# Kernel optimization log

Measured on AMD Instinct MI355X. Metric: run time of the kernel, lower is better.

Reference implementation:

```python
import jax, jax.numpy as jnp
import numpy as np

B, C, H, W = 2, 256, 64, 64
D = 4  # max dilation ring


def _offsets():
    offs = [(0, 0)]
    for s in range(1, D + 1):
        for a in (-s, 0, s):
            for b in (-s, 0, s):
                if a != 0 or b != 0:
                    offs.append((a, b))
    return np.array(offs, dtype=np.int32)  # (33, 2)


def setup_inputs() -> dict:
    key = jax.random.key(0)
    k1, k2, k3, k4 = jax.random.split(key, 4)
    scale = 1.0 / np.sqrt(C)
    return {
        "Ft": jax.random.normal(k1, (B, C, H, W), dtype=jnp.float32),
        "Ft_epsilon": jax.random.normal(k2, (B, C, H, W), dtype=jnp.float32),
        "Wf": jax.random.normal(k3, (256, C), dtype=jnp.float32) * scale,
        "bf": jnp.zeros((256,), dtype=jnp.float32),
        "Wg": jax.random.normal(k4, (256, C), dtype=jnp.float32) * scale,
        "bg": jnp.zeros((256,), dtype=jnp.float32),
    }


def reference(Ft, Ft_epsilon, Wf, bf, Wg, bg):
    # 1x1 conv embeddings
    Ef = jnp.einsum("bchw,oc->bohw", Ft, Wf) + bf[None, :, None, None]          # f(Ft)
    Eg = jnp.einsum("bchw,oc->bohw", Ft_epsilon, Wg) + bg[None, :, None, None]  # g(Ft_eps)

    offs = _offsets()                                  # (K,2), K=33
    dx = jnp.asarray(offs[:, 0])[:, None, None]        # (K,1,1)
    dy = jnp.asarray(offs[:, 1])[:, None, None]
    xs = jnp.arange(H)[None, :, None] + dx             # (K,H,1)
    ys = jnp.arange(W)[None, None, :] + dy             # (K,1,W)
    valid = ((xs >= 0) & (xs < H)) & ((ys >= 0) & (ys < W))  # (K,H,W)
    xc = jnp.clip(xs, 0, H - 1)
    yc = jnp.clip(ys, 0, W - 1)

    # gather neighbor embeddings and features: (B,C,K,H,W)
    Ef_n = Ef[:, :, xc, yc]
    Ft_n = Ft[:, :, xc, yc]

    # affinity of center embedding with each neighbor embedding
    aff = jnp.einsum("bchw,bckhw->bkhw", Eg, Ef_n)     # (B,K,H,W)
    aff = jnp.where(valid[None], aff, -jnp.inf)        # clip out-of-bounds neighbors
    w = jax.nn.softmax(aff, axis=1)                    # (B,K,H,W); center always valid

    out = jnp.einsum("bkhw,bckhw->bchw", w, Ft_n)      # (B,C,H,W)
    return out
```

## Files before the change

### kernel.cpp

```cpp
#include <hip/hip_runtime.h>
#include <math.h>

typedef __attribute__((ext_vector_type(4))) float f4;

__device__ __forceinline__ int iclamp(int x, int lo, int hi) { return min(max(x, lo), hi); }

__device__ constexpr int DXC[33] = {0, -1,-1,-1,0,0,1,1,1, -2,-2,-2,0,0,2,2,2, -3,-3,-3,0,0,3,3,3, -4,-4,-4,0,0,4,4,4};
__device__ constexpr int DYC[33] = {0, -1,0,1,-1,1,-1,0,1, -2,0,2,-2,2,-2,0,2, -3,0,3,-3,3,-3,0,3, -4,0,4,-4,4,-4,0,4};

__global__ __launch_bounds__(256) void mat_M(
    const float* __restrict__ Wf, const float* __restrict__ Wg,
    const float* __restrict__ bg, float* __restrict__ M, float* __restrict__ r)
{
    __shared__ float Sf[32][33], Sg[32][33];
    __shared__ float Rs[32][9];
    const int c1b = blockIdx.x * 32, c2b = blockIdx.y * 32;
    const int tid = threadIdx.x;
    const int tx = tid & 15, ty = tid >> 4;
    float acc[2][2] = {};
    for (int ko = 0; ko < 256; ko += 32) {
        #pragma unroll
        for (int i = 0; i < 4; ++i) {
            int f = i * 256 + tid;
            int o = f >> 5, c = f & 31;
            Sf[o][c] = Wf[(ko + o) * 256 + c1b + c];
            Sg[o][c] = Wg[(ko + o) * 256 + c2b + c];
        }
        __syncthreads();
        #pragma unroll
        for (int o = 0; o < 32; ++o) {
            float f0 = Sf[o][ty * 2], f1 = Sf[o][ty * 2 + 1];
            float g0 = Sg[o][tx * 2], g1 = Sg[o][tx * 2 + 1];
            acc[0][0] += f0 * g0; acc[0][1] += f0 * g1;
            acc[1][0] += f1 * g0; acc[1][1] += f1 * g1;
        }
        __syncthreads();
    }
    #pragma unroll
    for (int i = 0; i < 2; ++i)
        #pragma unroll
        for (int j = 0; j < 2; ++j)
            M[(size_t)(c1b + ty * 2 + i) * 256 + c2b + tx * 2 + j] = acc[i][j];

    if (blockIdx.y == 0) {
        const int c1l = tid & 31, og = tid >> 5;
        float s = 0.f;
        #pragma unroll 8
        for (int o = og * 32; o < og * 32 + 32; ++o)
            s += Wf[o * 256 + c1b + c1l] * bg[o];
        Rs[c1l][og] = s;
        __syncthreads();
        if (tid < 32) {
            float t = 0.f;
            #pragma unroll
            for (int j = 0; j < 8; ++j) t += Rs[tid][j];
            r[c1b + tid] = t;
        }
    }
}

__global__ __launch_bounds__(256, 2) void gemm_G(
    const float* __restrict__ M, const float* __restrict__ r,
    const float* __restrict__ X0, float* __restrict__ G)
{
    __shared__ float As[2][32][132];
    __shared__ float Bs[2][32][64];

    const int bn = blockIdx.x, bm = blockIdx.y, b = blockIdx.z;
    const float* X = X0 + (size_t)b * 256 * 4096;
    float* E = G + (size_t)b * 256 * 4096;

    const int tid = threadIdx.x;
    const int tn = tid & 15, tm = tid >> 4;
    const int m0 = bm * 128, n0 = bn * 64;

    float acc[8][4] = {};
    f4 areg[4], breg[2];

    auto loadA = [&](int kk) {
        #pragma unroll
        for (int i = 0; i < 4; ++i) {
            int f = i * 256 + tid, m = f >> 3, cq = f & 7;
            areg[i] = *(const f4*)&M[(m0 + m) * 256 + kk + cq * 4];
        }
    };
    auto loadB = [&](int kk) {
        #pragma unroll
        for (int i = 0; i < 2; ++i) {
            int f = i * 256 + tid, c = f >> 4, n4 = f & 15;
            breg[i] = *(const f4*)&X[(size_t)(kk + c) * 4096 + n0 + n4 * 4];
        }
    };
    auto storeLDS = [&](int buf) {
        #pragma unroll
        for (int i = 0; i < 4; ++i) {
            int f = i * 256 + tid, m = f >> 3, cq = f & 7;
            As[buf][cq * 4 + 0][m] = areg[i].x;
            As[buf][cq * 4 + 1][m] = areg[i].y;
            As[buf][cq * 4 + 2][m] = areg[i].z;
            As[buf][cq * 4 + 3][m] = areg[i].w;
        }
        #pragma unroll
        for (int i = 0; i < 2; ++i) {
            int f = i * 256 + tid, c = f >> 4, n4 = f & 15;
            *(f4*)&Bs[buf][c][n4 * 4] = breg[i];
        }
    };

    loadA(0); loadB(0); storeLDS(0);
    __syncthreads();

    for (int ch = 0; ch < 8; ++ch) {
        const int buf = ch & 1;
        if (ch < 7) { loadA((ch + 1) * 32); loadB((ch + 1) * 32); }
        #pragma unroll 4
        for (int k = 0; k < 32; ++k) {
            f4 a0 = *(const f4*)&As[buf][k][tm * 8];
            f4 a1 = *(const f4*)&As[buf][k][tm * 8 + 4];
            f4 bb = *(const f4*)&Bs[buf][k][tn * 4];
            #pragma unroll
            for (int ii = 0; ii < 4; ++ii)
                #pragma unroll
                for (int jj = 0; jj < 4; ++jj) {
                    acc[ii][jj]     += a0[ii] * bb[jj];
                    acc[4 + ii][jj] += a1[ii] * bb[jj];
                }
        }
        if (ch < 7) storeLDS(buf ^ 1);
        __syncthreads();
    }

    #pragma unroll
    for (int rr = 0; rr < 8; ++rr) {
        int o = m0 + tm * 8 + rr;
        float bvs = r[o];
        f4 v = { acc[rr][0] + bvs, acc[rr][1] + bvs, acc[rr][2] + bvs, acc[rr][3] + bvs };
        *(f4*)&E[(size_t)o * 4096 + n0 + tn * 4] = v;
    }
}

template<int K0, int NK>
__device__ __forceinline__ void aff_accum(const float* __restrict__ base, float* __restrict__ aff)
{
    #pragma unroll
    for (int ch = 0; ch < 8; ++ch) {
        float eg = base[(72 + ch) * 72];
        #pragma unroll
        for (int j = 0; j < NK; ++j) {
            constexpr int kk0 = K0;
            int k = kk0 + j;
            aff[j] += eg * base[((DXC[k] + 4) * 8 + ch) * 72 + DYC[k]];
        }
    }
}

__global__ __launch_bounds__(256, 2) void aff_part(
    const float* __restrict__ Ftg, const float* __restrict__ Gc,
    float* __restrict__ part)
{
    __shared__ float L[2][10 * 8 * 72];

    const int h = blockIdx.x, b = blockIdx.y, cseg = blockIdx.z;
    const int tid = threadIdx.x;
    const int w = tid & 63, kg = tid >> 6;
    const size_t plane = (size_t)b * 256 * 4096;
    const float* FtB = Ftg + plane;
    const float* GB  = Gc + plane;
    const int cbase = cseg * 64;

    int hr[10];
    #pragma unroll
    for (int d = 0; d < 10; ++d) hr[d] = (d < 9) ? iclamp(h + d - 4, 0, 63) : h;

    f4 vreg[5]; float sreg[3];

    auto load_rnd = [&](int rr) {
        const int c0 = cbase + rr * 8;
        #pragma unroll
        for (int i = 0; i < 5; ++i) {
            int f = i * 256 + tid, d = f >> 7, rem = f & 127, ch = rem >> 4, c4 = rem & 15;
            const float* src = (d < 9) ? FtB : GB;
            vreg[i] = *(const f4*)&src[(size_t)(c0 + ch) * 4096 + hr[d] * 64 + c4 * 4];
        }
        #pragma unroll
        for (int i = 0; i < 3; ++i) {
            int e = i * 256 + tid;
            if (e < 640) {
                int row = e >> 3, sc = e & 7, d = row >> 3, ch = row & 7;
                int wsrc = (sc < 4) ? 0 : 63;
                const float* src = (d < 9) ? FtB : GB;
                sreg[i] = src[(size_t)(c0 + ch) * 4096 + hr[d] * 64 + wsrc];
            }
        }
    };
    auto store_rnd = [&](int buf) {
        float* Lb = L[buf];
        #pragma unroll
        for (int i = 0; i < 5; ++i) {
            int f = i * 256 + tid, d = f >> 7, rem = f & 127, ch = rem >> 4, c4 = rem & 15;
            *(f4*)&Lb[(d * 8 + ch) * 72 + 4 + c4 * 4] = vreg[i];
        }
        #pragma unroll
        for (int i = 0; i < 3; ++i) {
            int e = i * 256 + tid;
            if (e < 640) {
                int row = e >> 3, sc = e & 7, d = row >> 3, ch = row & 7;
                int col = (sc < 4) ? sc : (64 + sc);
                Lb[(d * 8 + ch) * 72 + col] = sreg[i];
            }
        }
    };

    float aff[9] = {0.f,0.f,0.f,0.f,0.f,0.f,0.f,0.f,0.f};

    load_rnd(0); store_rnd(0);
    for (int rr = 0; rr < 8; ++rr) {
        if (rr < 7) load_rnd(rr + 1);
        __syncthreads();
        const float* base = &L[rr & 1][4 + w];
        switch (kg) {
            case 0: aff_accum<0, 9>(base, aff); break;
            case 1: aff_accum<9, 8>(base, aff); break;
            case 2: aff_accum<17, 8>(base, aff); break;
            default: aff_accum<25, 8>(base, aff); break;
        }
        if (rr < 7) store_rnd((rr + 1) & 1);
    }

    const int k0 = (kg == 0) ? 0 : (kg == 1) ? 9 : (kg == 2) ? 17 : 25;
    const int nk = (kg == 0) ? 9 : 8;
    float* pB = part + (((size_t)cseg * 2 + b) * 33) * 4096 + h * 64 + w;
    for (int j = 0; j < nk; ++j) pB[(size_t)(k0 + j) * 4096] = aff[j];
}

__global__ __launch_bounds__(256, 2) void out_kernel(
    const float* __restrict__ part, const float* __restrict__ Ft,
    float* __restrict__ out)
{
    __shared__ float L[2][9 * 8 * 72];

    const int h = blockIdx.x, b = blockIdx.y, cseg = blockIdx.z;
    const int tid = threadIdx.x;
    const int w = tid & 63, cg = tid >> 6;
    const size_t plane = (size_t)b * 256 * 4096;
    const float* FtB = Ft + plane;
    float* outB = out + plane;
    const int cbase = cseg * 64;
    const int p = h * 64 + w;

    int hr[9];
    #pragma unroll
    for (int d = 0; d < 9; ++d) hr[d] = iclamp(h + d - 4, 0, 63);

    f4 vreg[5]; float sreg[3];

    auto load_rnd = [&](int rr) {
        const int c0 = cbase + rr * 8;
        #pragma unroll
        for (int i = 0; i < 5; ++i) {
            int f = i * 256 + tid;
            if (f < 1152) {
                int d = f >> 7, rem = f & 127, ch = rem >> 4, c4 = rem & 15;
                vreg[i] = *(const f4*)&FtB[(size_t)(c0 + ch) * 4096 + hr[d] * 64 + c4 * 4];
            }
        }
        #pragma unroll
        for (int i = 0; i < 3; ++i) {
            int e = i * 256 + tid;
            if (e < 576) {
                int row = e >> 3, sc = e & 7, d = row >> 3, ch = row & 7;
                int wsrc = (sc < 4) ? 0 : 63;
                sreg[i] = FtB[(size_t)(c0 + ch) * 4096 + hr[d] * 64 + wsrc];
            }
        }
    };
    auto store_rnd = [&](int buf) {
        float* Lb = L[buf];
        #pragma unroll
        for (int i = 0; i < 5; ++i) {
            int f = i * 256 + tid;
            if (f < 1152) {
                int d = f >> 7, rem = f & 127, ch = rem >> 4, c4 = rem & 15;
                *(f4*)&Lb[(d * 8 + ch) * 72 + 4 + c4 * 4] = vreg[i];
            }
        }
        #pragma unroll
        for (int i = 0; i < 3; ++i) {
            int e = i * 256 + tid;
            if (e < 576) {
                int row = e >> 3, sc = e & 7, d = row >> 3, ch = row & 7;
                int col = (sc < 4) ? sc : (64 + sc);
                Lb[(d * 8 + ch) * 72 + col] = sreg[i];
            }
        }
    };

    load_rnd(0);

    float wv[33];
    {
        constexpr size_t CS = (size_t)2 * 33 * 4096;
        const float* pB = part + ((size_t)b * 33) * 4096 + p;
        float mx = -INFINITY;
        #pragma unroll
        for (int k = 0; k < 33; ++k) {
            size_t off = (size_t)k * 4096;
            float s = pB[off] + pB[CS + off] + pB[2 * CS + off] + pB[3 * CS + off];
            bool valid = ((unsigned)(h + DXC[k]) < 64u) && ((unsigned)(w + DYC[k]) < 64u);
            wv[k] = valid ? s : -INFINITY;
            mx = fmaxf(mx, wv[k]);
        }
        float ssum = 0.f;
        #pragma unroll
        for (int k = 0; k < 33; ++k) { float e = __expf(wv[k] - mx); wv[k] = e; ssum += e; }
        float inv = 1.0f / ssum;
        #pragma unroll
        for (int k = 0; k < 33; ++k) wv[k] *= inv;
    }

    store_rnd(0);
    for (int rr = 0; rr < 8; ++rr) {
        if (rr < 7) load_rnd(rr + 1);
        __syncthreads();
        const float* base = &L[rr & 1][4 + w];
        #pragma unroll
        for (int u = 0; u < 2; ++u) {
            const float* b2 = base + (cg * 2 + u) * 72;
            float o = 0.f;
            #pragma unroll
            for (int k = 0; k < 33; ++k)
                o += wv[k] * b2[(DXC[k] + 4) * 576 + DYC[k]];
            int c = cbase + rr * 8 + cg * 2 + u;
            outB[(size_t)c * 4096 + p] = o;
        }
        if (rr < 7) store_rnd((rr + 1) & 1);
    }
}

extern "C" void kernel_launch(void* const* d_in, const int* in_sizes, int n_in,
                              void* d_out, int out_size, void* d_ws, size_t ws_size,
                              hipStream_t stream) {
    const float* Ft  = (const float*)d_in[0];
    const float* FtE = (const float*)d_in[1];
    const float* Wf  = (const float*)d_in[2];
    const float* bf  = (const float*)d_in[3];
    const float* Wg  = (const float*)d_in[4];
    const float* bg  = (const float*)d_in[5];
    float* out = (float*)d_out;
    (void)bf;

    float* G    = (float*)d_ws;
    float* part = G + (size_t)2 * 256 * 4096;
    float* Mw   = part + (size_t)4 * 2 * 33 * 4096;
    float* rw   = Mw + 256 * 256;

    hipLaunchKernelGGL(mat_M, dim3(8, 8), dim3(256), 0, stream,
                       Wf, Wg, bg, Mw, rw);
    hipLaunchKernelGGL(gemm_G, dim3(64, 2, 2), dim3(256), 0, stream,
                       Mw, rw, FtE, G);
    hipLaunchKernelGGL(aff_part, dim3(64, 2, 4), dim3(256), 0, stream,
                       Ft, G, part);
    hipLaunchKernelGGL(out_kernel, dim3(64, 2, 4), dim3(256), 0, stream,
                       part, Ft, out);
}
```

Before: 143.7 us.

## Fuse four kernels into one cooperative persistent kernel with grid syncs

Replaces the four separate launches (weight product, embedding GEMM, affinity partials, output) with a single cooperative kernel of 512 blocks that runs each phase in turn, separated by grid.sync. The GEMM tile is shrunk from 128 to 64 rows so every phase maps onto the same 512-block grid. This is meant to remove launch gaps and inter-kernel drain between phases. The cost is grid-wide barriers, the need for all 512 blocks to be co-resident, and a smaller GEMM tile with less register reuse. If the cooperative launch fails, it falls back to four separate kernels.

Measured after the change: 320.6 us. 2.23x slower.

```diff
diff --git a/kernel.cpp b/kernel.cpp
--- a/kernel.cpp
+++ b/kernel.cpp
@@ -1,5 +1,8 @@
 #include <hip/hip_runtime.h>
+#include <hip/hip_cooperative_groups.h>
 #include <math.h>
+
+namespace cg = cooperative_groups;
 
 typedef __attribute__((ext_vector_type(4))) float f4;
 
@@ -8,21 +11,21 @@
 __device__ constexpr int DXC[33] = {0, -1,-1,-1,0,0,1,1,1, -2,-2,-2,0,0,2,2,2, -3,-3,-3,0,0,3,3,3, -4,-4,-4,0,0,4,4,4};
 __device__ constexpr int DYC[33] = {0, -1,0,1,-1,1,-1,0,1, -2,0,2,-2,2,-2,0,2, -3,0,3,-3,3,-3,0,3, -4,0,4,-4,4,-4,0,4};
 
-__global__ __launch_bounds__(256) void mat_M(
-    const float* __restrict__ Wf, const float* __restrict__ Wg,
-    const float* __restrict__ bg, float* __restrict__ M, float* __restrict__ r)
-{
-    __shared__ float Sf[32][33], Sg[32][33];
-    __shared__ float Rs[32][9];
-    const int c1b = blockIdx.x * 32, c2b = blockIdx.y * 32;
-    const int tid = threadIdx.x;
+__device__ __forceinline__ void phase_M(
+    float* LDSf, const float* __restrict__ Wf, const float* __restrict__ Wg,
+    const float* __restrict__ bg, float* __restrict__ M, float* __restrict__ r,
+    int bid, int tid)
+{
+    float (*Sf)[33] = (float(*)[33])LDSf;
+    float (*Sg)[33] = (float(*)[33])(LDSf + 32 * 33);
+    float (*Rs)[9]  = (float(*)[9])(LDSf + 2 * 32 * 33);
+    const int c1b = (bid & 7) * 32, c2b = (bid >> 3) * 32;
     const int tx = tid & 15, ty = tid >> 4;
     float acc[2][2] = {};
     for (int ko = 0; ko < 256; ko += 32) {
         #pragma unroll
         for (int i = 0; i < 4; ++i) {
-            int f = i * 256 + tid;
-            int o = f >> 5, c = f & 31;
+            int f = i * 256 + tid, o = f >> 5, c = f & 31;
             Sf[o][c] = Wf[(ko + o) * 256 + c1b + c];
             Sg[o][c] = Wg[(ko + o) * 256 + c2b + c];
         }
@@ -42,7 +45,7 @@
         for (int j = 0; j < 2; ++j)
             M[(size_t)(c1b + ty * 2 + i) * 256 + c2b + tx * 2 + j] = acc[i][j];
 
-    if (blockIdx.y == 0) {
+    if ((bid >> 3) == 0) {
         const int c1l = tid & 31, og = tid >> 5;
         float s = 0.f;
         #pragma unroll 8
@@ -59,27 +62,23 @@
     }
 }
 
-__global__ __launch_bounds__(256, 2) void gemm_G(
-    const float* __restrict__ M, const float* __restrict__ r,
-    const float* __restrict__ X0, float* __restrict__ G)
-{
-    __shared__ float As[2][32][132];
-    __shared__ float Bs[2][32][64];
-
-    const int bn = blockIdx.x, bm = blockIdx.y, b = blockIdx.z;
-    const float* X = X0 + (size_t)b * 256 * 4096;
+__device__ __forceinline__ void phase_gemm(
+    float* LDSf, const float* __restrict__ M, const float* __restrict__ r,
+    const float* __restrict__ FtE, float* __restrict__ G,
+    int bn, int bm, int b, int tid)
+{
+    float (*As)[68] = (float(*)[68])LDSf;
+    float (*Bs)[64] = (float(*)[64])(LDSf + 64 * 68);
+    const float* X = FtE + (size_t)b * 256 * 4096;
     float* E = G + (size_t)b * 256 * 4096;
-
-    const int tid = threadIdx.x;
     const int tn = tid & 15, tm = tid >> 4;
-    const int m0 = bm * 128, n0 = bn * 64;
-
-    float acc[8][4] = {};
-    f4 areg[4], breg[2];
+    const int m0 = bm * 64, n0 = bn * 64;
+    float acc[4][4] = {};
+    f4 areg[2], breg[2];
 
     auto loadA = [&](int kk) {
         #pragma unroll
-        for (int i = 0; i < 4; ++i) {
+        for (int i = 0; i < 2; ++i) {
             int f = i * 256 + tid, m = f >> 3, cq = f & 7;
             areg[i] = *(const f4*)&M[(m0 + m) * 256 + kk + cq * 4];
         }
@@ -93,48 +92,43 @@
     };
     auto storeLDS = [&](int buf) {
         #pragma unroll
-        for (int i = 0; i < 4; ++i) {
+        for (int i = 0; i < 2; ++i) {
             int f = i * 256 + tid, m = f >> 3, cq = f & 7;
-            As[buf][cq * 4 + 0][m] = areg[i].x;
-            As[buf][cq * 4 + 1][m] = areg[i].y;
-            As[buf][cq * 4 + 2][m] = areg[i].z;
-            As[buf][cq * 4 + 3][m] = areg[i].w;
+            As[buf * 32 + cq * 4 + 0][m] = areg[i].x;
+            As[buf * 32 + cq * 4 + 1][m] = areg[i].y;
+            As[buf * 32 + cq * 4 + 2][m] = areg[i].z;
+            As[buf * 32 + cq * 4 + 3][m] = areg[i].w;
         }
         #pragma unroll
         for (int i = 0; i < 2; ++i) {
             int f = i * 256 + tid, c = f >> 4, n4 = f & 15;
-            *(f4*)&Bs[buf][c][n4 * 4] = breg[i];
+            *(f4*)&Bs[buf * 32 + c][n4 * 4] = breg[i];
         }
     };
 
     loadA(0); loadB(0); storeLDS(0);
     __syncthreads();
-
     for (int ch = 0; ch < 8; ++ch) {
         const int buf = ch & 1;
         if (ch < 7) { loadA((ch + 1) * 32); loadB((ch + 1) * 32); }
         #pragma unroll 4
         for (int k = 0; k < 32; ++k) {
-            f4 a0 = *(const f4*)&As[buf][k][tm * 8];
-            f4 a1 = *(const f4*)&As[buf][k][tm * 8 + 4];
-            f4 bb = *(const f4*)&Bs[buf][k][tn * 4];
+            f4 a  = *(const f4*)&As[buf * 32 + k][tm * 4];
+            f4 bb = *(const f4*)&Bs[buf * 32 + k][tn * 4];
             #pragma unroll
             for (int ii = 0; ii < 4; ++ii)
                 #pragma unroll
-                for (int jj = 0; jj < 4; ++jj) {
-                    acc[ii][jj]     += a0[ii] * bb[jj];
-                    acc[4 + ii][jj] += a1[ii] * bb[jj];
-                }
+                for (int jj = 0; jj < 4; ++jj)
+                    acc[ii][jj] += a[ii] * bb[jj];
         }
         if (ch < 7) storeLDS(buf ^ 1);
         __syncthreads();
     }
-
-    #pragma unroll
-    for (int rr = 0; rr < 8; ++rr) {
-        int o = m0 + tm * 8 + rr;
+    #pragma unroll
+    for (int ii = 0; ii < 4; ++ii) {
+        int o = m0 + tm * 4 + ii;
         float bvs = r[o];
-        f4 v = { acc[rr][0] + bvs, acc[rr][1] + bvs, acc[rr][2] + bvs, acc[rr][3] + bvs };
+        f4 v = { acc[ii][0] + bvs, acc[ii][1] + bvs, acc[ii][2] + bvs, acc[ii][3] + bvs };
         *(f4*)&E[(size_t)o * 4096 + n0 + tn * 4] = v;
     }
 }
@@ -154,14 +148,11 @@
     }
 }
 
-__global__ __launch_bounds__(256, 2) void aff_part(
-    const float* __restrict__ Ftg, const float* __restrict__ Gc,
-    float* __restrict__ part)
-{
-    __shared__ float L[2][10 * 8 * 72];
-
-    const int h = blockIdx.x, b = blockIdx.y, cseg = blockIdx.z;
-    const int tid = threadIdx.x;
+__device__ __forceinline__ void phase_aff(
+    float* LDSf, const float* __restrict__ Ftg, const float* __restrict__ Gc,
+    float* __restrict__ part, int h, int b, int cseg, int tid)
+{
+    float (*L)[5760] = (float(*)[5760])LDSf;
     const int w = tid & 63, kg = tid >> 6;
     const size_t plane = (size_t)b * 256 * 4096;
     const float* FtB = Ftg + plane;
@@ -230,17 +221,16 @@
     const int k0 = (kg == 0) ? 0 : (kg == 1) ? 9 : (kg == 2) ? 17 : 25;
     const int nk = (kg == 0) ? 9 : 8;
     float* pB = part + (((size_t)cseg * 2 + b) * 33) * 4096 + h * 64 + w;
-    for (int j = 0; j < nk; ++j) pB[(size_t)(k0 + j) * 4096] = aff[j];
-}
-
-__global__ __launch_bounds__(256, 2) void out_kernel(
-    const float* __restrict__ part, const float* __restrict__ Ft,
-    float* __restrict__ out)
-{
-    __shared__ float L[2][9 * 8 * 72];
-
-    const int h = blockIdx.x, b = blockIdx.y, cseg = blockIdx.z;
-    const int tid = threadIdx.x;
+    #pragma unroll
+    for (int j = 0; j < 9; ++j)
+        if (j < nk) pB[(size_t)(k0 + j) * 4096] = aff[j];
+}
+
+__device__ __forceinline__ void phase_out(
+    float* LDSf, const float* __restrict__ part, const float* __restrict__ Ft,
+    float* __restrict__ out, int h, int b, int cseg, int tid)
+{
+    float (*L)[5184] = (float(*)[5184])LDSf;
     const int w = tid & 63, cg = tid >> 6;
     const size_t plane = (size_t)b * 256 * 4096;
     const float* FtB = Ft + plane;
@@ -335,6 +325,60 @@
         }
         if (rr < 7) store_rnd((rr + 1) & 1);
     }
+}
+
+__global__ __launch_bounds__(256, 2) void fused_all(
+    const float* __restrict__ Wf, const float* __restrict__ Wg,
+    const float* __restrict__ bg, const float* __restrict__ Ft,
+    const float* __restrict__ FtE, float* __restrict__ Mw, float* __restrict__ rw,
+    float* __restrict__ G, float* __restrict__ part, float* __restrict__ out)
+{
+    __shared__ float LDS[11520];
+    cg::grid_group grid = cg::this_grid();
+    const int bid = blockIdx.x, tid = threadIdx.x;
+
+    if (bid < 64) phase_M(LDS, Wf, Wg, bg, Mw, rw, bid, tid);
+    grid.sync();
+    phase_gemm(LDS, Mw, rw, FtE, G, bid & 63, (bid >> 6) & 3, bid >> 8, tid);
+    grid.sync();
+    phase_aff(LDS, Ft, G, part, bid & 63, (bid >> 6) & 1, bid >> 7, tid);
+    grid.sync();
+    phase_out(LDS, part, Ft, out, bid & 63, (bid >> 6) & 1, bid >> 7, tid);
+}
+
+__global__ __launch_bounds__(256) void k_M(
+    const float* __restrict__ Wf, const float* __restrict__ Wg,
+    const float* __restrict__ bg, float* __restrict__ M, float* __restrict__ r)
+{
+    __shared__ float LDS[2 * 32 * 33 + 32 * 9];
+    phase_M(LDS, Wf, Wg, bg, M, r, blockIdx.x, threadIdx.x);
+}
+
+__global__ __launch_bounds__(256, 2) void k_gemm(
+    const float* __restrict__ M, const float* __restrict__ r,
+    const float* __restrict__ FtE, float* __restrict__ G)
+{
+    __shared__ float LDS[64 * 68 + 64 * 64];
+    const int bid = blockIdx.x;
+    phase_gemm(LDS, M, r, FtE, G, bid & 63, (bid >> 6) & 3, bid >> 8, threadIdx.x);
+}
+
+__global__ __launch_bounds__(256, 2) void k_aff(
+    const float* __restrict__ Ft, const float* __restrict__ G,
+    float* __restrict__ part)
+{
+    __shared__ float LDS[2 * 5760];
+    const int bid = blockIdx.x;
+    phase_aff(LDS, Ft, G, part, bid & 63, (bid >> 6) & 1, bid >> 7, threadIdx.x);
+}
+
+__global__ __launch_bounds__(256, 2) void k_out(
+    const float* __restrict__ part, const float* __restrict__ Ft,
+    float* __restrict__ out)
+{
+    __shared__ float LDS[2 * 5184];
+    const int bid = blockIdx.x;
+    phase_out(LDS, part, Ft, out, bid & 63, (bid >> 6) & 1, bid >> 7, threadIdx.x);
 }
 
 extern "C" void kernel_launch(void* const* d_in, const int* in_sizes, int n_in,
@@ -354,12 +398,15 @@
     float* Mw   = part + (size_t)4 * 2 * 33 * 4096;
     float* rw   = Mw + 256 * 256;
 
-    hipLaunchKernelGGL(mat_M, dim3(8, 8), dim3(256), 0, stream,
-                       Wf, Wg, bg, Mw, rw);
-    hipLaunchKernelGGL(gemm_G, dim3(64, 2, 2), dim3(256), 0, stream,
-                       Mw, rw, FtE, G);
-    hipLaunchKernelGGL(aff_part, dim3(64, 2, 4), dim3(256), 0, stream,
-                       Ft, G, part);
-    hipLaunchKernelGGL(out_kernel, dim3(64, 2, 4), dim3(256), 0, stream,
-                       part, Ft, out);
-}
+    void* args[10] = { (void*)&Wf, (void*)&Wg, (void*)&bg, (void*)&Ft, (void*)&FtE,
+                       (void*)&Mw, (void*)&rw, (void*)&G, (void*)&part, (void*)&out };
+    hipError_t err = hipLaunchCooperativeKernel(
+        reinterpret_cast<const void*>(&fused_all), dim3(512), dim3(256),
+        args, 0, stream);
+    if (err != hipSuccess) {
+        hipLaunchKernelGGL(k_M,    dim3(64),  dim3(256), 0, stream, Wf, Wg, bg, Mw, rw);
+        hipLaunchKernelGGL(k_gemm, dim3(512), dim3(256), 0, stream, Mw, rw, FtE, G);
+        hipLaunchKernelGGL(k_aff,  dim3(512), dim3(256), 0, stream, Ft, G, part);
+        hipLaunchKernelGGL(k_out,  dim3(512), dim3(256), 0, stream, part, Ft, out);
+    }
+}
```
